# Kernel tuning notes

Hardware: AMD Instinct MI355X
Metric: run time of the kernel (lower is better)

## Reference

```python
import jax, jax.numpy as jnp
import numpy as np

H, W = 512, 512          # image_size
N = 10000                # num gaussians (point cloud size)
NUM_VIEWS = 4
PATCH = 40               # original uses arange(v-20, v+20) -> 40px window


def setup_inputs() -> dict:
    key = jax.random.key(0)
    ks = jax.random.split(key, 6)
    means = jax.random.normal(ks[0], (N, 3), dtype=jnp.float32) * 0.5
    log_scales = jnp.log(0.1) + 0.1 * jax.random.normal(ks[1], (N, 3), dtype=jnp.float32)
    q = jax.random.normal(ks[2], (N, 4), dtype=jnp.float32)
    quats = q / jnp.linalg.norm(q, axis=1, keepdims=True)
    shs = jax.random.normal(ks[3], (N, 3, 16), dtype=jnp.float32) * 0.1  # (sh_degree+1)^2 = 16
    opacities = jnp.full((N, 1), 0.5, dtype=jnp.float32)
    # Camera poses: small yaw sweep looking at the origin from z=+5 so points project in-frame.
    poses = []
    for a in np.linspace(-0.1, 0.1, NUM_VIEWS):
        Rm = np.array([[np.cos(a), 0.0, np.sin(a)],
                       [0.0, 1.0, 0.0],
                       [-np.sin(a), 0.0, np.cos(a)]], dtype=np.float32)
        P = np.eye(4, dtype=np.float32)
        P[:3, :3] = Rm
        P[:3, 3] = np.array([0.0, 0.0, 5.0], dtype=np.float32)
        poses.append(P)
    poses = jnp.asarray(np.stack(poses))
    intrinsics = jnp.asarray(np.array([[500.0, 0.0, 256.0],
                                       [0.0, 500.0, 256.0],
                                       [0.0, 0.0, 1.0]], dtype=np.float32))
    return {"poses": poses, "intrinsics": intrinsics, "means": means,
            "log_scales": log_scales, "quats": quats, "shs": shs, "opacities": opacities}


def _quat_to_mat(q):
    # q: (N,4) wxyz -> (N,3,3), same formula as the torch module
    w, x, y, z = q[:, 0], q[:, 1], q[:, 2], q[:, 3]
    r0 = jnp.stack([1 - 2 * (y * y + z * z), 2 * (x * y - w * z), 2 * (x * z + w * y)], -1)
    r1 = jnp.stack([2 * (x * y + w * z), 1 - 2 * (x * x + z * z), 2 * (y * z - w * x)], -1)
    r2 = jnp.stack([2 * (x * z - w * y), 2 * (y * z + w * x), 1 - 2 * (x * x + y * y)], -1)
    return jnp.stack([r0, r1, r2], -2)


def _render_view(pose, K, means, log_scales, quats, shs, opacities):
    Rm = pose[:3, :3]
    t = pose[:3, 3]
    p_cam = means @ Rm.T + t                      # (N,3)
    p_proj = p_cam @ K.T                          # (N,3)
    uv = p_proj[:, :2] / (p_proj[:, 2:3] + 1e-8)  # (N,2)
    u = jnp.trunc(uv[:, 0]).astype(jnp.int32)     # int(uv) truncation as in python int()
    v = jnp.trunc(uv[:, 1]).astype(jnp.int32)
    valid = (p_cam[:, 2] >= 0.1) & (u >= 0) & (u < W) & (v >= 0) & (v < H)

    scales = jnp.exp(log_scales)                  # (N,3); module uses scale (not scale^2)
    Rg = _quat_to_mat(quats)                      # (N,3,3)
    cov = jnp.einsum('nij,nj,nkj->nik', Rg, scales, Rg)  # R diag(s) R^T
    a, b = cov[:, 0, 0], cov[:, 0, 1]
    c, d = cov[:, 1, 0], cov[:, 1, 1]
    det = a * d - b * c
    inv = jnp.stack([jnp.stack([d, -b], -1), jnp.stack([-c, a], -1)], -2) / det[:, None, None]  # inverse of cov[:2,:2]

    off = jnp.arange(PATCH, dtype=jnp.int32) - PATCH // 2  # -20..19, matches arange(v-20, v+20)
    yy = jnp.broadcast_to(v[:, None, None] + off[None, :, None], (N, PATCH, PATCH))
    xx = jnp.broadcast_to(u[:, None, None] + off[None, None, :], (N, PATCH, PATCH))
    pos = jnp.stack([xx, yy], -1).astype(jnp.float32) - uv[:, None, None, :]  # (N,40,40,2)
    expo = -0.5 * jnp.einsum('nyxi,nij,nyxj->nyx', pos, inv, pos)
    g = jnp.exp(jnp.clip(expo, -10.0, 0.0))

    inb = (yy >= 0) & (yy < H) & (xx >= 0) & (xx < W)
    mask = valid[:, None, None] & inb & (g > 0.001)

    color = jax.nn.sigmoid(shs[:, :, 0])          # (N,3)
    op = jax.nn.sigmoid(opacities)                # (N,1)
    contrib = jnp.where(mask, g, 0.0)[..., None] * (op * color)[:, None, None, :]  # (N,40,40,3)

    image = jnp.zeros((H, W, 3), jnp.float32)
    image = image.at[jnp.clip(yy, 0, H - 1), jnp.clip(xx, 0, W - 1)].add(contrib)
    return image


def reference(poses, intrinsics, means, log_scales, quats, shs, opacities):
    # loop over a small fixed number of views (matches forward's per-view loop)
    imgs = [_render_view(poses[i], intrinsics, means, log_scales, quats, shs, opacities)
            for i in range(NUM_VIEWS)]
    return jnp.stack(imgs)  # (num_views, H, W, 3)
```

## Files before the change

kernel.cpp:

```cpp
#include <hip/hip_runtime.h>

#define IMG_H 512
#define IMG_W 512
#define NGAUSS 10000
#define N_VIEWS 4
#define PATCH 40

#define QMAX 13.815511f

#define BLOCK_T 1024
#define BAND_ROWS 8
#define NBANDS_IMG (IMG_H / BAND_ROWS)
#define NBLOCKS (N_VIEWS * NBANDS_IMG)
#define QCAP 3072
#define IMG_FLOATS (BAND_ROWS * IMG_W * 3)

__device__ __forceinline__ float fast_sigmoid(float x) {
    return 1.0f / (1.0f + __expf(-x));
}

__global__ __launch_bounds__(BLOCK_T) void gs_band_kernel(
    const float* __restrict__ poses,
    const float* __restrict__ Km,
    const float* __restrict__ means,
    const float* __restrict__ log_scales,
    const float* __restrict__ quats,
    const float* __restrict__ shs,
    const float* __restrict__ opac,
    float* __restrict__ out)
{
    __shared__ float s_img[IMG_FLOATS];
    __shared__ int   s_queue[QCAP];
    __shared__ int   s_qn;

    const int view = blockIdx.x >> 6;
    const int y0   = (blockIdx.x & 63) << 3;
    const int tid  = threadIdx.x;

    float4* img4 = reinterpret_cast<float4*>(s_img);
    #pragma unroll
    for (int i = 0; i < IMG_FLOATS / 4 / BLOCK_T; ++i)
        img4[i * BLOCK_T + tid] = make_float4(0.f, 0.f, 0.f, 0.f);
    if (tid == 0) s_qn = 0;
    __syncthreads();

    const float* P = poses + view * 16;
    const float P0 = P[0], P1 = P[1], P2  = P[2],  P3  = P[3];
    const float P4 = P[4], P5 = P[5], P6  = P[6],  P7  = P[7];
    const float P8 = P[8], P9 = P[9], P10 = P[10], P11 = P[11];
    const float K0 = Km[0], K1 = Km[1], K2 = Km[2];
    const float K3 = Km[3], K4 = Km[4], K5 = Km[5];
    const float K6 = Km[6], K7 = Km[7], K8 = Km[8];

    for (int n = tid; n < NGAUSS; n += BLOCK_T) {
        const float m0 = means[n * 3 + 0];
        const float m1 = means[n * 3 + 1];
        const float m2 = means[n * 3 + 2];

        const float Xc = P0 * m0 + P1 * m1 + P2  * m2 + P3;
        const float Yc = P4 * m0 + P5 * m1 + P6  * m2 + P7;
        const float Zc = P8 * m0 + P9 * m1 + P10 * m2 + P11;

        const float ppx = K0 * Xc + K1 * Yc + K2 * Zc;
        const float ppy = K3 * Xc + K4 * Yc + K5 * Zc;
        const float ppz = K6 * Xc + K7 * Yc + K8 * Zc;

        const float rcp = 1.0f / (ppz + 1e-8f);
        const float uvx = ppx * rcp;
        const float uvy = ppy * rcp;

        const int u = (int)uvx;
        const int v = (int)uvy;

        if (!((Zc >= 0.1f) && (u >= 0) && (u < IMG_W) && (v >= 0) && (v < IMG_H)))
            continue;

        const float ls0 = log_scales[n * 3 + 0];
        const float ls1 = log_scales[n * 3 + 1];
        const float ls2 = log_scales[n * 3 + 2];
        const float ry  = sqrtf(QMAX * __expf(fmaxf(fmaxf(ls0, ls1), ls2))) + 0.5f;

        const int ylo = max((int)ceilf (uvy - ry), max(v - PATCH / 2, 0));
        const int yhi = min((int)floorf(uvy + ry), min(v + PATCH / 2 - 1, IMG_H - 1));
        if (ylo > yhi || ylo > y0 + (BAND_ROWS - 1) || yhi < y0)
            continue;

        const int idx = atomicAdd(&s_qn, 1);
        if (idx < QCAP) s_queue[idx] = n;
    }
    __syncthreads();

    const int qn = min(s_qn, QCAP);

    for (int i = tid; i < qn; i += BLOCK_T) {
        const int n = s_queue[i];

        const float m0 = means[n * 3 + 0];
        const float m1 = means[n * 3 + 1];
        const float m2 = means[n * 3 + 2];

        const float4 qv = *reinterpret_cast<const float4*>(quats + n * 4);
        const float qw = qv.x, qx = qv.y, qy = qv.z, qz = qv.w;
        const float R00 = 1.0f - 2.0f * (qy * qy + qz * qz);
        const float R01 = 2.0f * (qx * qy - qw * qz);
        const float R02 = 2.0f * (qx * qz + qw * qy);
        const float R10 = 2.0f * (qx * qy + qw * qz);
        const float R11 = 1.0f - 2.0f * (qx * qx + qz * qz);
        const float R12 = 2.0f * (qy * qz - qw * qx);

        const float s0 = __expf(log_scales[n * 3 + 0]);
        const float s1 = __expf(log_scales[n * 3 + 1]);
        const float s2 = __expf(log_scales[n * 3 + 2]);

        const float a  = R00 * R00 * s0 + R01 * R01 * s1 + R02 * R02 * s2;
        const float b  = R00 * R10 * s0 + R01 * R11 * s1 + R02 * R12 * s2;
        const float dd = R10 * R10 * s0 + R11 * R11 * s1 + R12 * R12 * s2;

        const float det = a * dd - b * b;
        const float i00 =  dd / det;
        const float i01 = -b  / det;
        const float i11 =  a  / det;

        const float rx = sqrtf(QMAX * a)  + 0.5f;
        const float ry = sqrtf(QMAX * dd) + 0.5f;

        const float op = fast_sigmoid(opac[n]);
        const float w0 = op * fast_sigmoid(shs[n * 48 +  0]);
        const float w1 = op * fast_sigmoid(shs[n * 48 + 16]);
        const float w2 = op * fast_sigmoid(shs[n * 48 + 32]);

        const float Xc = P0 * m0 + P1 * m1 + P2  * m2 + P3;
        const float Yc = P4 * m0 + P5 * m1 + P6  * m2 + P7;
        const float Zc = P8 * m0 + P9 * m1 + P10 * m2 + P11;
        const float ppx = K0 * Xc + K1 * Yc + K2 * Zc;
        const float ppy = K3 * Xc + K4 * Yc + K5 * Zc;
        const float ppz = K6 * Xc + K7 * Yc + K8 * Zc;
        const float rcp = 1.0f / (ppz + 1e-8f);
        const float uvx = ppx * rcp;
        const float uvy = ppy * rcp;
        const int u = (int)uvx;
        const int v = (int)uvy;

        const int xlo = max((int)ceilf (uvx - rx), max(u - PATCH / 2, 0));
        const int xhi = min((int)floorf(uvx + rx), min(u + PATCH / 2 - 1, IMG_W - 1));
        const int ylo = max(max((int)ceilf (uvy - ry), max(v - PATCH / 2, 0)), y0);
        const int yhi = min(min((int)floorf(uvy + ry),
                                min(v + PATCH / 2 - 1, IMG_H - 1)),
                            y0 + (BAND_ROWS - 1));

        for (int yy = ylo; yy <= yhi; ++yy) {
            const float dy = (float)yy - uvy;
            const float qy2  = i11 * dy * dy;
            const float qy1  = 2.0f * i01 * dy;
            float* row = s_img + (size_t)(yy - y0) * (IMG_W * 3);
            for (int xx = xlo; xx <= xhi; ++xx) {
                const float dx = (float)xx - uvx;
                const float q  = i00 * dx * dx + qy1 * dx + qy2;
                const float g  = __expf(fminf(fmaxf(-0.5f * q, -10.0f), 0.0f));
                if (g > 0.001f) {
                    atomicAdd(row + xx * 3 + 0, g * w0);
                    atomicAdd(row + xx * 3 + 1, g * w1);
                    atomicAdd(row + xx * 3 + 2, g * w2);
                }
            }
        }
    }
    __syncthreads();

    float4* o4 = reinterpret_cast<float4*>(
        out + ((size_t)view * IMG_H + y0) * (IMG_W * 3));
    #pragma unroll
    for (int i = 0; i < IMG_FLOATS / 4 / BLOCK_T; ++i)
        o4[i * BLOCK_T + tid] = img4[i * BLOCK_T + tid];
}

extern "C" void kernel_launch(void* const* d_in, const int* in_sizes, int n_in,
                              void* d_out, int out_size, void* d_ws, size_t ws_size,
                              hipStream_t stream) {
    const float* poses      = (const float*)d_in[0];
    const float* intrinsics = (const float*)d_in[1];
    const float* means      = (const float*)d_in[2];
    const float* log_scales = (const float*)d_in[3];
    const float* quats      = (const float*)d_in[4];
    const float* shs        = (const float*)d_in[5];
    const float* opac       = (const float*)d_in[6];
    float* out = (float*)d_out;

    gs_band_kernel<<<NBLOCKS, BLOCK_T, 0, stream>>>(
        poses, intrinsics, means, log_scales, quats, shs, opac, out);
}
```

Before: 92.56 us.

## Switch from scatter-atomic splatting to per-strip gather with binned gaussian lists

Replaces the per-gaussian scatter into a shared-memory image band, which used LDS float atomics, with a gather approach. Gaussians are binned into 16-column strips during culling. Each thread then owns one column and four rows and accumulates contributions in registers from its strip's list before writing straight to global memory. This removes the shared-memory atomics and the band zero/copy, but it caps per-strip lists at 256 and the queue at 1300, which risks silently dropping gaussians if more overlap a band. It also adds per-pixel culling and bound checks.

New measurement: 131.3 us. +41.8%, slower.

```diff
diff --git a/kernel.cpp b/kernel.cpp
--- a/kernel.cpp
+++ b/kernel.cpp
@@ -12,8 +12,9 @@
 #define BAND_ROWS 8
 #define NBANDS_IMG (IMG_H / BAND_ROWS)
 #define NBLOCKS (N_VIEWS * NBANDS_IMG)
-#define QCAP 3072
-#define IMG_FLOATS (BAND_ROWS * IMG_W * 3)
+#define NSUB 32
+#define QCAP 1300
+#define CAP_ST 256
 
 __device__ __forceinline__ float fast_sigmoid(float x) {
     return 1.0f / (1.0f + __expf(-x));
@@ -29,18 +30,18 @@
     const float* __restrict__ opac,
     float* __restrict__ out)
 {
-    __shared__ float s_img[IMG_FLOATS];
-    __shared__ int   s_queue[QCAP];
-    __shared__ int   s_qn;
+    __shared__ float4 s_p0[QCAP];
+    __shared__ float4 s_p1[QCAP];
+    __shared__ int    s_qid[QCAP];
+    __shared__ unsigned short s_list[NSUB * CAP_ST];
+    __shared__ int    s_ln[NSUB];
+    __shared__ int    s_qn;
 
     const int view = blockIdx.x >> 6;
     const int y0   = (blockIdx.x & 63) << 3;
     const int tid  = threadIdx.x;
 
-    float4* img4 = reinterpret_cast<float4*>(s_img);
-    #pragma unroll
-    for (int i = 0; i < IMG_FLOATS / 4 / BLOCK_T; ++i)
-        img4[i * BLOCK_T + tid] = make_float4(0.f, 0.f, 0.f, 0.f);
+    if (tid < NSUB) s_ln[tid] = 0;
     if (tid == 0) s_qn = 0;
     __syncthreads();
 
@@ -78,22 +79,33 @@
         const float ls0 = log_scales[n * 3 + 0];
         const float ls1 = log_scales[n * 3 + 1];
         const float ls2 = log_scales[n * 3 + 2];
-        const float ry  = sqrtf(QMAX * __expf(fmaxf(fmaxf(ls0, ls1), ls2))) + 0.5f;
-
-        const int ylo = max((int)ceilf (uvy - ry), max(v - PATCH / 2, 0));
-        const int yhi = min((int)floorf(uvy + ry), min(v + PATCH / 2 - 1, IMG_H - 1));
+        const float rub = sqrtf(QMAX * __expf(fmaxf(fmaxf(ls0, ls1), ls2))) + 0.5f;
+
+        const int ylo = max((int)ceilf (uvy - rub), max(v - PATCH / 2, 0));
+        const int yhi = min((int)floorf(uvy + rub), min(v + PATCH / 2 - 1, IMG_H - 1));
         if (ylo > yhi || ylo > y0 + (BAND_ROWS - 1) || yhi < y0)
             continue;
 
-        const int idx = atomicAdd(&s_qn, 1);
-        if (idx < QCAP) s_queue[idx] = n;
+        const int xlo = max((int)ceilf (uvx - rub), max(u - PATCH / 2, 0));
+        const int xhi = min((int)floorf(uvx + rub), min(u + PATCH / 2 - 1, IMG_W - 1));
+        if (xlo > xhi) continue;
+
+        const int qidx = atomicAdd(&s_qn, 1);
+        if (qidx >= QCAP) continue;
+        s_qid[qidx] = n;
+
+        const int st0 = xlo >> 4, st1 = xhi >> 4;
+        for (int st = st0; st <= st1; ++st) {
+            const int li = atomicAdd(&s_ln[st], 1);
+            if (li < CAP_ST) s_list[st * CAP_ST + li] = (unsigned short)qidx;
+        }
     }
     __syncthreads();
 
     const int qn = min(s_qn, QCAP);
 
     for (int i = tid; i < qn; i += BLOCK_T) {
-        const int n = s_queue[i];
+        const int n = s_qid[i];
 
         const float m0 = means[n * 3 + 0];
         const float m1 = means[n * 3 + 1];
@@ -121,9 +133,6 @@
         const float i01 = -b  / det;
         const float i11 =  a  / det;
 
-        const float rx = sqrtf(QMAX * a)  + 0.5f;
-        const float ry = sqrtf(QMAX * dd) + 0.5f;
-
         const float op = fast_sigmoid(opac[n]);
         const float w0 = op * fast_sigmoid(shs[n * 48 +  0]);
         const float w1 = op * fast_sigmoid(shs[n * 48 + 16]);
@@ -136,42 +145,61 @@
         const float ppy = K3 * Xc + K4 * Yc + K5 * Zc;
         const float ppz = K6 * Xc + K7 * Yc + K8 * Zc;
         const float rcp = 1.0f / (ppz + 1e-8f);
-        const float uvx = ppx * rcp;
-        const float uvy = ppy * rcp;
-        const int u = (int)uvx;
-        const int v = (int)uvy;
-
-        const int xlo = max((int)ceilf (uvx - rx), max(u - PATCH / 2, 0));
-        const int xhi = min((int)floorf(uvx + rx), min(u + PATCH / 2 - 1, IMG_W - 1));
-        const int ylo = max(max((int)ceilf (uvy - ry), max(v - PATCH / 2, 0)), y0);
-        const int yhi = min(min((int)floorf(uvy + ry),
-                                min(v + PATCH / 2 - 1, IMG_H - 1)),
-                            y0 + (BAND_ROWS - 1));
-
-        for (int yy = ylo; yy <= yhi; ++yy) {
-            const float dy = (float)yy - uvy;
-            const float qy2  = i11 * dy * dy;
-            const float qy1  = 2.0f * i01 * dy;
-            float* row = s_img + (size_t)(yy - y0) * (IMG_W * 3);
-            for (int xx = xlo; xx <= xhi; ++xx) {
-                const float dx = (float)xx - uvx;
-                const float q  = i00 * dx * dx + qy1 * dx + qy2;
-                const float g  = __expf(fminf(fmaxf(-0.5f * q, -10.0f), 0.0f));
-                if (g > 0.001f) {
-                    atomicAdd(row + xx * 3 + 0, g * w0);
-                    atomicAdd(row + xx * 3 + 1, g * w1);
-                    atomicAdd(row + xx * 3 + 2, g * w2);
-                }
+
+        s_p0[i] = make_float4(ppx * rcp, ppy * rcp, i00, i01);
+        s_p1[i] = make_float4(i11, w0, w1, w2);
+    }
+    __syncthreads();
+
+    const int st   = tid >> 5;
+    const int l    = tid & 31;
+    const int col  = (st << 4) + (l & 15);
+    const int rsel = l >> 4;
+    const float fx = (float)col;
+
+    float accR[4] = {0.f, 0.f, 0.f, 0.f};
+    float accG[4] = {0.f, 0.f, 0.f, 0.f};
+    float accB[4] = {0.f, 0.f, 0.f, 0.f};
+
+    const int ln = min(s_ln[st], CAP_ST);
+    for (int k = 0; k < ln; ++k) {
+        const int qi = s_list[st * CAP_ST + k];
+        const float4 p0 = s_p0[qi];
+        const float4 p1 = s_p1[qi];
+
+        const float dx   = fx - p0.x;
+        const float det2 = p0.z * p1.x - p0.w * p0.w;
+        if (dx * dx * det2 >= QMAX * p1.x) continue;
+
+        const int u = (int)p0.x;
+        const int v = (int)p0.y;
+        const bool colok = (col >= u - PATCH / 2) & (col <= u + PATCH / 2 - 1);
+
+        const float A = p0.z * dx * dx;
+        const float B = 2.0f * p0.w * dx;
+
+        #pragma unroll
+        for (int r = 0; r < 4; ++r) {
+            const int py = y0 + rsel + (r << 1);
+            const float dy = (float)py - p0.y;
+            const float q  = A + dy * (B + p1.x * dy);
+            const float g  = __expf(fminf(fmaxf(-0.5f * q, -10.0f), 0.0f));
+            const bool ok = colok & (g > 0.001f)
+                          & (py >= v - PATCH / 2) & (py <= v + PATCH / 2 - 1);
+            if (ok) {
+                accR[r] += g * p1.y;
+                accG[r] += g * p1.z;
+                accB[r] += g * p1.w;
             }
         }
     }
-    __syncthreads();
-
-    float4* o4 = reinterpret_cast<float4*>(
-        out + ((size_t)view * IMG_H + y0) * (IMG_W * 3));
+
     #pragma unroll
-    for (int i = 0; i < IMG_FLOATS / 4 / BLOCK_T; ++i)
-        o4[i * BLOCK_T + tid] = img4[i * BLOCK_T + tid];
+    for (int r = 0; r < 4; ++r) {
+        const int py = y0 + rsel + (r << 1);
+        float* o = out + (((size_t)view * IMG_H + py) * IMG_W + col) * 3;
+        o[0] = accR[r]; o[1] = accG[r]; o[2] = accB[r];
+    }
 }
 
 extern "C" void kernel_launch(void* const* d_in, const int* in_sizes, int n_in,
```
